# Kernel tuning notes

Hardware: AMD Instinct MI355X
Metric: run time of the kernel (lower is better)

The kernel has to match this reference:

```python
import jax, jax.numpy as jnp
import numpy as np
from functools import partial

H = 768          # hidden_size (bert-base)
S = 256          # seq_len, forced by pool Linear(256*H -> H)
V = 30522        # vocab_size
NUM_TAGS = 2
B = 32


def _lstm_layer(x, w_ih, w_hh, b_ih, b_hh):
    # x: (B, S, I); torch weight layout: w_ih (4H, I), w_hh (4H, H), gate order i,f,g,o
    b, _, _ = x.shape
    h0 = jnp.zeros((b, H), x.dtype)
    c0 = jnp.zeros((b, H), x.dtype)
    bias = b_ih + b_hh

    def step(carry, xt):
        h, c = carry
        gates = xt @ w_ih.T + h @ w_hh.T + bias          # (B, 4H)
        i, f, g, o = jnp.split(gates, 4, axis=-1)
        i = jax.nn.sigmoid(i)
        f = jax.nn.sigmoid(f)
        g = jnp.tanh(g)
        o = jax.nn.sigmoid(o)
        c = f * c + i * g
        h = o * jnp.tanh(c)
        return (h, c), h

    _, hs = jax.lax.scan(step, (h0, c0), x.transpose(1, 0, 2))  # hs: (S, B, H)
    return hs.transpose(1, 0, 2)


def setup_inputs() -> dict:
    key = jax.random.key(0)
    ks = jax.random.split(key, 16)
    sc = 0.02
    inp = {
        "input_ids": jax.random.randint(ks[0], (B, S), 0, V, dtype=jnp.int32),
        "attention_mask": jnp.ones((B, S), jnp.int32),
        "token_type_ids": jnp.zeros((B, S), jnp.int32),
        "seq_label": jax.random.randint(ks[1], (B, NUM_TAGS), 0, 2, dtype=jnp.int32),
        "entity_ids": jax.random.randint(ks[2], (B, S), 0, 2, dtype=jnp.int32),
        "embed_table": jax.random.normal(ks[3], (V, H), jnp.float32) * sc,
        "w_ih0": jax.random.normal(ks[4], (4 * H, H), jnp.float32) * sc,
        "w_hh0": jax.random.normal(ks[5], (4 * H, H), jnp.float32) * sc,
        "b_ih0": jnp.zeros((4 * H,), jnp.float32),
        "b_hh0": jnp.zeros((4 * H,), jnp.float32),
        "w_ih1": jax.random.normal(ks[6], (4 * H, H), jnp.float32) * sc,
        "w_hh1": jax.random.normal(ks[7], (4 * H, H), jnp.float32) * sc,
        "b_ih1": jnp.zeros((4 * H,), jnp.float32),
        "b_hh1": jnp.zeros((4 * H,), jnp.float32),
        "pool_w": jax.random.normal(ks[8], (S * H, H), jnp.float32) * 0.002,
        "pool_b": jnp.zeros((H,), jnp.float32),
        "lin_w": jax.random.normal(ks[9], (H, NUM_TAGS), jnp.float32) * sc,
        "lin_b": jnp.zeros((NUM_TAGS,), jnp.float32),
    }
    return inp


def reference(input_ids, attention_mask, token_type_ids, seq_label, entity_ids,
              embed_table, w_ih0, w_hh0, b_ih0, b_hh0, w_ih1, w_hh1, b_ih1, b_hh1,
              pool_w, pool_b, lin_w, lin_b):
    x = embed_table[input_ids]                              # (B, S, H)
    out = _lstm_layer(x, w_ih0, w_hh0, b_ih0, b_hh0)        # layer 1
    out = _lstm_layer(out, w_ih1, w_hh1, b_ih1, b_hh1)      # layer 2 -> (B, S, H)

    seq_out = out.reshape(out.shape[0], -1) @ pool_w + pool_b   # (B, H)

    # batched version of the per-sample loop:
    # entity_out = tokens * (entity_ids == 1); concat seq_out row; global max over tokens
    mask = (entity_ids == 1).astype(out.dtype)[:, :, None]      # (B, S, 1)
    entity_out = out * mask                                     # (B, S, H)
    batch_out = jnp.maximum(entity_out.max(axis=1), seq_out)    # adaptive_max_pool1d(size=1)

    logits = batch_out @ lin_w + lin_b                          # (B, num_tags)

    # BCEWithLogitsLoss (dropout in eval mode = identity), numerically stable
    y = seq_label.astype(logits.dtype)
    loss = jnp.mean(jnp.maximum(logits, 0) - logits * y + jnp.log1p(jnp.exp(-jnp.abs(logits))))
    return (loss, logits)
```

## Files before the change

kernel.cpp:

```cpp
#include <hip/hip_runtime.h>
#include <hip/hip_bf16.h>
#include <stdint.h>

constexpr int Hh  = 768;
constexpr int Ss  = 256;
constexpr int Bb  = 32;
constexpr int NWGL = 96;
constexpr int UPW8 = Hh / NWGL;
constexpr int LCW  = 4 * UPW8;
constexpr int WPAD = Hh + 8;
constexpr int CPT  = 256;
constexpr int PB   = 40;
constexpr int NCH  = 3;

typedef short bf16x8 __attribute__((ext_vector_type(8)));
typedef float f32x4  __attribute__((ext_vector_type(4)));
typedef float f32x2  __attribute__((ext_vector_type(2)));
typedef uint32_t u32x4 __attribute__((ext_vector_type(4)));

__device__ __forceinline__ unsigned short f2bf(float f) {
  union { float f; uint32_t u; } v; v.f = f;
  uint32_t u = v.u;
  return (unsigned short)((u + 0x7FFFu + ((u >> 16) & 1u)) >> 16);
}
__device__ __forceinline__ float bf2f(unsigned short h) {
  union { uint32_t u; float f; } v; v.u = ((uint32_t)h) << 16; return v.f;
}

__global__ __launch_bounds__(256) void k_embed(const int* __restrict__ ids,
                                               const float* __restrict__ table,
                                               unsigned short* __restrict__ x_bf) {
  int row = blockIdx.x;
  int b = row / Ss, s = row - b * Ss;
  int id  = ids[row];
  const float* src = table + (size_t)id * Hh;
  unsigned short* dst = x_bf + ((size_t)s * Bb + b) * Hh;
  for (int j = threadIdx.x; j < Hh; j += 256) dst[j] = f2bf(src[j]);
}

__global__ __launch_bounds__(256) void k_lstm2(
    const unsigned short* __restrict__ x_bf,
    const float* __restrict__ w_ih0, const float* __restrict__ w_hh0,
    const float* __restrict__ w_ih1, const float* __restrict__ w_hh1,
    const float* __restrict__ b_ih0, const float* __restrict__ b_hh0,
    const float* __restrict__ b_ih1, const float* __restrict__ b_hh1,
    unsigned short* __restrict__ hseq1,
    unsigned short* __restrict__ hseq2,
    unsigned int* __restrict__ sync) {
  __shared__ __align__(16) unsigned short Whh[LCW * WPAD];
  __shared__ __align__(16) unsigned short Wih[LCW * WPAD];
  __shared__ __align__(16) unsigned short hbuf[2][16][8];
  __shared__ __align__(16) float gsum[2][2][16][33];
  __shared__ int prodf[2], consf[2];
  __shared__ int stepC, stepP;

  const int wgid = blockIdx.x;
  const int tid = threadIdx.x;
  const int lane = tid & 63, w = tid >> 6;
  unsigned int* cnt1 = sync;
  unsigned int* cnt2 = sync + Ss * CPT;

  const int layer = wgid >= NWGL;
  const int wg = layer ? wgid - NWGL : wgid;
  const int u0 = wg * UPW8;
  const int bkt = wg & 15;

  if (tid < 2) { prodf[tid] = 0; consf[tid] = -1; }
  if (tid == 2) stepC = 0;
  if (tid == 3) stepP = 0;

  {
    const float* whsrc = layer ? w_hh1 : w_hh0;
    const float* wisrc = layer ? w_ih1 : w_ih0;
    for (int cch = tid; cch < LCW * 96; cch += 256) {
      int row = cch / 96, kc = cch - row * 96;
      int gi = row >> 3, u = row & 7;
      const float* sp = whsrc + ((size_t)gi * Hh + u0 + u) * Hh + kc * 8;
      float4 va = ((const float4*)sp)[0], vb = ((const float4*)sp)[1];
      bf16x8 pk;
      pk[0] = (short)f2bf(va.x); pk[1] = (short)f2bf(va.y);
      pk[2] = (short)f2bf(va.z); pk[3] = (short)f2bf(va.w);
      pk[4] = (short)f2bf(vb.x); pk[5] = (short)f2bf(vb.y);
      pk[6] = (short)f2bf(vb.z); pk[7] = (short)f2bf(vb.w);
      *(bf16x8*)&Whh[row * WPAD + kc * 8] = pk;
      const float* sp2 = wisrc + ((size_t)gi * Hh + u0 + u) * Hh + kc * 8;
      float4 vc = ((const float4*)sp2)[0], vd = ((const float4*)sp2)[1];
      bf16x8 pk2;
      pk2[0] = (short)f2bf(vc.x); pk2[1] = (short)f2bf(vc.y);
      pk2[2] = (short)f2bf(vc.z); pk2[3] = (short)f2bf(vc.w);
      pk2[4] = (short)f2bf(vd.x); pk2[5] = (short)f2bf(vd.y);
      pk2[6] = (short)f2bf(vd.z); pk2[7] = (short)f2bf(vd.w);
      *(bf16x8*)&Wih[row * WPAD + kc * 8] = pk2;
    }
  }
  __syncthreads();

  const int l15 = lane & 15, kq = lane >> 4;
  const bool lo8 = (l15 < 8);
  volatile int* scp = &stepC;
  volatile int* spp = &stepP;

  if (w >= 2) {
    const int bh = w - 2;
    const int brow = bh * 16 + l15;
    for (int t = 0; t < Ss; ++t) {
      if (layer) {
        if (w == 2) {
          const unsigned int* bk = cnt1 + (size_t)t * CPT;
          for (;;) {
            unsigned v = 12;
            if (lane < 16)
              v = __hip_atomic_load(bk + lane * 16, __ATOMIC_RELAXED, __HIP_MEMORY_SCOPE_AGENT);
            if (__all(v >= 12u)) break;
            __builtin_amdgcn_s_sleep(2);
          }
          asm volatile("" ::: "memory");
          if (lane == 0) *spp = t + 1;
          asm volatile("s_waitcnt lgkmcnt(0)" ::: "memory");
        } else {
          while (*spp < t + 1) __builtin_amdgcn_s_sleep(1);
          asm volatile("" ::: "memory");
        }
      }
      const unsigned short* ap = (layer ? hseq1 : x_bf)
                               + ((size_t)t * Bb + brow) * Hh + kq * 8;
      bf16x8 areg[24];
      #pragma unroll
      for (int kk = 0; kk < 24; ++kk) areg[kk] = *(const bf16x8*)(ap + kk * 32);
      f32x4 aI[2][2];
      #pragma unroll
      for (int nt = 0; nt < 2; ++nt) {
        aI[nt][0] = (f32x4){0.f,0.f,0.f,0.f}; aI[nt][1] = (f32x4){0.f,0.f,0.f,0.f};
        const int c = nt * 16 + l15;
        #pragma unroll
        for (int kk = 0; kk < 24; ++kk) {
          bf16x8 bfr = *(const bf16x8*)&Wih[c * WPAD + kk * 32 + kq * 8];
          aI[nt][kk & 1] = __builtin_amdgcn_mfma_f32_16x16x32_bf16(areg[kk], bfr, aI[nt][kk & 1], 0, 0, 0);
        }
      }
      while (__hip_atomic_load(&consf[bh], __ATOMIC_RELAXED, __HIP_MEMORY_SCOPE_WORKGROUP) < t - 1)
        __builtin_amdgcn_s_sleep(0);
      const int par = t & 1;
      #pragma unroll
      for (int nt = 0; nt < 2; ++nt)
        #pragma unroll
        for (int r = 0; r < 4; ++r)
          gsum[par][bh][kq * 4 + r][nt * 16 + l15] = aI[nt][0][r] + aI[nt][1][r];
      __hip_atomic_store(&prodf[bh], t + 1, __ATOMIC_RELEASE, __HIP_MEMORY_SCOPE_WORKGROUP);
    }
    return;
  }

  const int bh = w;
  const int brow = bh * 16 + l15;
  const float k1 = lo8 ? 2.f : 1.f;
  const float m1 = lo8 ? 2.f : 1.f;
  const float d1 = lo8 ? -1.f : 0.f;

  float bl[2];
  #pragma unroll
  for (int nt = 0; nt < 2; ++nt) {
    int c = nt * 16 + l15;
    int gcol = (c >> 3) * Hh + u0 + (c & 7);
    bl[nt] = layer ? (b_ih1[gcol] + b_hh1[gcol]) : (b_ih0[gcol] + b_hh0[gcol]);
  }

  float cc[4] = {0.f, 0.f, 0.f, 0.f};
  unsigned short* hout = layer ? hseq2 : hseq1;
  unsigned int* mycnt = layer ? cnt2 : cnt1;

  for (int t = 0; t < Ss; ++t) {
    f32x4 aW[2][2];
    #pragma unroll
    for (int nt = 0; nt < 2; ++nt) {
      aW[nt][0] = (f32x4){0.f,0.f,0.f,0.f}; aW[nt][1] = (f32x4){0.f,0.f,0.f,0.f};
    }
    if (t > 0) {
      if (w == 0) {
        const unsigned int* bown = mycnt + (size_t)(t - 1) * CPT;
        for (;;) {
          unsigned v = 12;
          if (lane < 16)
            v = __hip_atomic_load(bown + lane * 16, __ATOMIC_RELAXED, __HIP_MEMORY_SCOPE_AGENT);
          if (__all(v >= 12u)) break;
          __builtin_amdgcn_s_sleep(2);
        }
        asm volatile("" ::: "memory");
        if (lane == 0) *scp = t;
        asm volatile("s_waitcnt lgkmcnt(0)" ::: "memory");
      } else {
        while (*scp < t) __builtin_amdgcn_s_sleep(1);
        asm volatile("" ::: "memory");
      }
      const unsigned short* ap = hout + ((size_t)(t - 1) * Bb + brow) * Hh + kq * 8;
      bf16x8 areg[24];
      #pragma unroll
      for (int kk = 0; kk < 24; ++kk) areg[kk] = *(const bf16x8*)(ap + kk * 32);
      #pragma unroll
      for (int nt = 0; nt < 2; ++nt) {
        const int c = nt * 16 + l15;
        #pragma unroll
        for (int kk = 0; kk < 24; ++kk) {
          bf16x8 bfr = *(const bf16x8*)&Whh[c * WPAD + kk * 32 + kq * 8];
          aW[nt][kk & 1] = __builtin_amdgcn_mfma_f32_16x16x32_bf16(areg[kk], bfr, aW[nt][kk & 1], 0, 0, 0);
        }
      }
    }

    float gin[2][4];
    {
      while (__hip_atomic_load(&prodf[bh], __ATOMIC_ACQUIRE, __HIP_MEMORY_SCOPE_WORKGROUP) < t + 1)
        __builtin_amdgcn_s_sleep(0);
      const int par = t & 1;
      #pragma unroll
      for (int nt = 0; nt < 2; ++nt)
        #pragma unroll
        for (int r = 0; r < 4; ++r)
          gin[nt][r] = gsum[par][bh][kq * 4 + r][nt * 16 + l15] + bl[nt];
      __hip_atomic_store(&consf[bh], t, __ATOMIC_RELEASE, __HIP_MEMORY_SCOPE_WORKGROUP);
    }

    float act0[4], act1[4];
    #pragma unroll
    for (int r = 0; r < 4; ++r) {
      float v0 = aW[0][0][r] + aW[0][1][r] + gin[0][r];
      act0[r] = 1.f / (1.f + __expf(-v0));
      float v1 = aW[1][0][r] + aW[1][1][r] + gin[1][r];
      act1[r] = m1 / (1.f + __expf(-k1 * v1)) + d1;
    }

    #pragma unroll
    for (int r = 0; r < 4; ++r) {
      float p0 = __shfl_xor(act0[r], 8);
      float p1 = __shfl_xor(act1[r], 8);
      float iv = lo8 ? act0[r] : p0;
      float fv = lo8 ? p0 : act0[r];
      float gv = lo8 ? act1[r] : p1;
      float ov = lo8 ? p1 : act1[r];
      float cn = fv * cc[r] + iv * gv;
      cc[r] = cn;
      float e = __expf(-2.f * cn);
      float hv = ov * (1.f - e) / (1.f + e);
      if (lo8) hbuf[w][kq * 4 + r][l15] = f2bf(hv);
    }
    asm volatile("s_waitcnt lgkmcnt(0)" ::: "memory");

    if (lane < 16) {
      const unsigned long long* hb = (const unsigned long long*)&hbuf[w][lane][0];
      unsigned long long x0 = hb[0], x1 = hb[1];
      unsigned long long* hp =
          (unsigned long long*)(hout + ((size_t)t * Bb + (bh * 16 + lane)) * Hh + u0);
      __hip_atomic_store(hp + 0, x0, __ATOMIC_RELAXED, __HIP_MEMORY_SCOPE_AGENT);
      __hip_atomic_store(hp + 1, x1, __ATOMIC_RELAXED, __HIP_MEMORY_SCOPE_AGENT);
    }
    asm volatile("s_waitcnt vmcnt(0)" ::: "memory");
    if (lane == 0) {
      unsigned int* cp = mycnt + (size_t)t * CPT + bkt * 16;
      (void)__hip_atomic_fetch_add(cp, 1u, __ATOMIC_RELAXED, __HIP_MEMORY_SCOPE_AGENT);
    }
  }
}

__global__ __launch_bounds__(256) void k_pool_partial(const unsigned short* __restrict__ hseq2,
                                                      const float* __restrict__ pw,
                                                      float* __restrict__ partial) {
  __shared__ __align__(16) unsigned short osm[Hh * PB];
  const int tid = threadIdx.x;
  const int s = blockIdx.x, nc = blockIdx.y;
  for (int b = 0; b < Bb; ++b) {
    const unsigned short* src = hseq2 + ((size_t)s * Bb + b) * Hh;
    for (int k = tid; k < Hh; k += 256) osm[k * PB + b] = src[k];
  }
  __syncthreads();
  f32x2 acc[16];
  #pragma unroll
  for (int bp = 0; bp < 16; ++bp) acc[bp] = (f32x2){0.f, 0.f};
  const float* pbase = pw + (size_t)s * Hh * Hh + nc * 256 + tid;
  #pragma unroll 4
  for (int k = 0; k < Hh; ++k) {
    float wv = pbase[(size_t)k * Hh];
    u32x4 h0 = *(const u32x4*)&osm[k * PB + 0];
    u32x4 h1 = *(const u32x4*)&osm[k * PB + 8];
    u32x4 h2 = *(const u32x4*)&osm[k * PB + 16];
    u32x4 h3 = *(const u32x4*)&osm[k * PB + 24];
    uint32_t hw[16] = {h0[0],h0[1],h0[2],h0[3], h1[0],h1[1],h1[2],h1[3],
                       h2[0],h2[1],h2[2],h2[3], h3[0],h3[1],h3[2],h3[3]};
    #pragma unroll
    for (int bp = 0; bp < 16; ++bp) {
      uint32_t pv = hw[bp];
      f32x2 ov;
      ov.x = __uint_as_float(pv << 16);
      ov.y = __uint_as_float(pv & 0xffff0000u);
      acc[bp] += ov * wv;
    }
  }
  float* pout = partial + (size_t)(s * NCH + nc) * (Bb * 256);
  #pragma unroll
  for (int bp = 0; bp < 16; ++bp) {
    pout[(size_t)(bp * 2 + 0) * 256 + tid] = acc[bp].x;
    pout[(size_t)(bp * 2 + 1) * 256 + tid] = acc[bp].y;
  }
}

__global__ __launch_bounds__(256) void k_pool_reduce(const float* __restrict__ partial,
                                                     const float* __restrict__ pool_b,
                                                     float* __restrict__ seq_out) {
  int i = blockIdx.x * 256 + threadIdx.x;
  int b = i / Hh, n = i - b * Hh;
  int nchunk = n >> 8, nn = n & 255;
  float acc = pool_b[n];
  const float* p = partial + (size_t)nchunk * (Bb * 256) + b * 256 + nn;
  #pragma unroll 8
  for (int t = 0; t < Ss; ++t) acc += p[(size_t)t * NCH * (Bb * 256)];
  seq_out[i] = acc;
}

__global__ __launch_bounds__(256) void k_entity_logits(const unsigned short* __restrict__ hseq2,
                                                       const float* __restrict__ seq_out,
                                                       const int* __restrict__ entity_ids,
                                                       const float* __restrict__ lin_w,
                                                       const float* __restrict__ lin_b,
                                                       float* __restrict__ logits_ws,
                                                       float* __restrict__ dlogits) {
  const int b = blockIdx.x, tid = threadIdx.x;
  float m0 = -1e30f, m1 = -1e30f, m2 = -1e30f;
  for (int s = 0; s < Ss; ++s) {
    bool e = entity_ids[b * Ss + s] == 1;
    const unsigned short* row = hseq2 + ((size_t)s * Bb + b) * Hh;
    float v0 = bf2f(row[tid]);
    float v1 = bf2f(row[256 + tid]);
    float v2 = bf2f(row[512 + tid]);
    v0 = e ? v0 : 0.f; v1 = e ? v1 : 0.f; v2 = e ? v2 : 0.f;
    m0 = fmaxf(m0, v0); m1 = fmaxf(m1, v1); m2 = fmaxf(m2, v2);
  }
  __shared__ float red[512];
  float p0 = 0.f, p1 = 0.f;
  float mm[3] = {m0, m1, m2};
  #pragma unroll
  for (int j = 0; j < 3; ++j) {
    int n = j * 256 + tid;
    float bo = fmaxf(mm[j], seq_out[b * Hh + n]);
    p0 += bo * lin_w[n * 2 + 0];
    p1 += bo * lin_w[n * 2 + 1];
  }
  red[tid] = p0; red[256 + tid] = p1;
  __syncthreads();
  for (int off = 128; off > 0; off >>= 1) {
    if (tid < off) { red[tid] += red[tid + off]; red[256 + tid] += red[256 + tid + off]; }
    __syncthreads();
  }
  if (tid == 0) {
    float l0 = red[0] + lin_b[0], l1 = red[256] + lin_b[1];
    logits_ws[b * 2] = l0; logits_ws[b * 2 + 1] = l1;
    dlogits[b * 2] = l0;  dlogits[b * 2 + 1] = l1;
  }
}

__global__ void k_loss(const float* __restrict__ logits, const int* __restrict__ lab,
                       float* __restrict__ dout) {
  __shared__ float red[64];
  int i = threadIdx.x;
  float l = logits[i];
  float y = (float)lab[i];
  red[i] = fmaxf(l, 0.f) - l * y + log1pf(__expf(-fabsf(l)));
  __syncthreads();
  for (int off = 32; off > 0; off >>= 1) {
    if (i < off) red[i] += red[i + off];
    __syncthreads();
  }
  if (i == 0) dout[0] = red[0] * (1.f / 64.f);
}

extern "C" void kernel_launch(void* const* d_in, const int* in_sizes, int n_in,
                              void* d_out, int out_size, void* d_ws, size_t ws_size,
                              hipStream_t stream) {
  const int*   input_ids  = (const int*)d_in[0];
  const int*   seq_label  = (const int*)d_in[3];
  const int*   entity_ids = (const int*)d_in[4];
  const float* embed      = (const float*)d_in[5];
  const float* w_ih0      = (const float*)d_in[6];
  const float* w_hh0      = (const float*)d_in[7];
  const float* b_ih0      = (const float*)d_in[8];
  const float* b_hh0      = (const float*)d_in[9];
  const float* w_ih1      = (const float*)d_in[10];
  const float* w_hh1      = (const float*)d_in[11];
  const float* b_ih1      = (const float*)d_in[12];
  const float* b_hh1      = (const float*)d_in[13];
  const float* pool_w     = (const float*)d_in[14];
  const float* pool_b     = (const float*)d_in[15];
  const float* lin_w      = (const float*)d_in[16];
  const float* lin_b      = (const float*)d_in[17];
  float* out = (float*)d_out;

  const size_t SZ_XO = (size_t)Bb * Ss * Hh * 2;
  const size_t SZ_SY = (size_t)2 * Ss * CPT * 4;
  char* ws = (char*)d_ws;
  size_t off = 0;
  unsigned short* x_bf   = (unsigned short*)(ws + off); off += SZ_XO;
  unsigned short* hseq1  = (unsigned short*)(ws + off); off += SZ_XO;
  unsigned short* hseq2  = (unsigned short*)(ws + off); off += SZ_XO;
  float*          seq_out= (float*)(ws + off);          off += (size_t)Bb * Hh * 4;
  float*          logits = (float*)(ws + off);          off += 1024;
  unsigned int*   syncb  = (unsigned int*)(ws + off);   off += SZ_SY;
  float*          partial = (float*)ws;

  hipMemsetAsync(syncb, 0, SZ_SY, stream);

  k_embed<<<Bb * Ss, 256, 0, stream>>>(input_ids, embed, x_bf);

  k_lstm2<<<2 * NWGL, 256, 0, stream>>>(x_bf, w_ih0, w_hh0, w_ih1, w_hh1,
                                        b_ih0, b_hh0, b_ih1, b_hh1,
                                        hseq1, hseq2, syncb);

  dim3 pgrid(Ss, NCH);
  k_pool_partial<<<pgrid, 256, 0, stream>>>(hseq2, pool_w, partial);
  k_pool_reduce<<<(Bb * Hh) / 256, 256, 0, stream>>>(partial, pool_b, seq_out);
  k_entity_logits<<<Bb, 256, 0, stream>>>(hseq2, seq_out, entity_ids, lin_w, lin_b,
                                          logits, out + 1);
  k_loss<<<1, 64, 0, stream>>>(logits, seq_label, out);
}
```

Before: 2.193 ms.

## Add dedicated polling wave for cross-WG sync and fuse pool-reduce/loss into logits

Adds a fifth wavefront per workgroup that solely polls the global step counters and publishes progress to LDS flags. The compute waves then spin on LDS with minimal sleep instead of one compute wave doing the global polling. Separately, the pool reduction and loss kernels are folded into the entity/logits kernel, with a last-block atomic counter computing the loss, which removes two launches. The cost is extra threads per block and a serial partial-sum reduction inside only 32 blocks.

```diff
diff --git a/kernel.cpp b/kernel.cpp
--- a/kernel.cpp
+++ b/kernel.cpp
@@ -38,7 +38,7 @@
   for (int j = threadIdx.x; j < Hh; j += 256) dst[j] = f2bf(src[j]);
 }
 
-__global__ __launch_bounds__(256) void k_lstm2(
+__global__ __launch_bounds__(320) void k_lstm2(
     const unsigned short* __restrict__ x_bf,
     const float* __restrict__ w_ih0, const float* __restrict__ w_hh0,
     const float* __restrict__ w_ih1, const float* __restrict__ w_hh1,
@@ -72,7 +72,7 @@
   {
     const float* whsrc = layer ? w_hh1 : w_hh0;
     const float* wisrc = layer ? w_ih1 : w_ih0;
-    for (int cch = tid; cch < LCW * 96; cch += 256) {
+    for (int cch = tid; cch < LCW * 96; cch += 320) {
       int row = cch / 96, kc = cch - row * 96;
       int gi = row >> 3, u = row & 7;
       const float* sp = whsrc + ((size_t)gi * Hh + u0 + u) * Hh + kc * 8;
@@ -99,28 +99,51 @@
   const bool lo8 = (l15 < 8);
   volatile int* scp = &stepC;
   volatile int* spp = &stepP;
+  unsigned int* mycnt = layer ? cnt2 : cnt1;
+
+  if (w == 4) {
+    if (layer) {
+      int tc = 1, tp = 0;
+      while (tc <= Ss || tp < Ss) {
+        bool c = true;
+        if (lane < 16 && tc <= Ss)
+          c = __hip_atomic_load(cnt2 + (size_t)(tc - 1) * CPT + lane * 16,
+                                __ATOMIC_RELAXED, __HIP_MEMORY_SCOPE_AGENT) >= 12u;
+        else if (lane >= 16 && lane < 32 && tp < Ss)
+          c = __hip_atomic_load(cnt1 + (size_t)tp * CPT + (lane - 16) * 16,
+                                __ATOMIC_RELAXED, __HIP_MEMORY_SCOPE_AGENT) >= 12u;
+        unsigned long long bal = __ballot(c);
+        bool ownok = (tc <= Ss) && ((bal & 0xFFFFull) == 0xFFFFull);
+        bool inok  = (tp < Ss) && (((bal >> 16) & 0xFFFFull) == 0xFFFFull);
+        asm volatile("" ::: "memory");
+        if (ownok) { if (lane == 0) *scp = tc; ++tc; }
+        if (inok)  { if (lane == 0) *spp = tp + 1; ++tp; }
+        if (!ownok && !inok) __builtin_amdgcn_s_sleep(1);
+      }
+    } else {
+      for (int tc = 1; tc <= Ss; ++tc) {
+        for (;;) {
+          unsigned v = 12;
+          if (lane < 16)
+            v = __hip_atomic_load(cnt1 + (size_t)(tc - 1) * CPT + lane * 16,
+                                  __ATOMIC_RELAXED, __HIP_MEMORY_SCOPE_AGENT);
+          if (__all(v >= 12u)) break;
+          __builtin_amdgcn_s_sleep(1);
+        }
+        asm volatile("" ::: "memory");
+        if (lane == 0) *scp = tc;
+      }
+    }
+    return;
+  }
 
   if (w >= 2) {
     const int bh = w - 2;
     const int brow = bh * 16 + l15;
     for (int t = 0; t < Ss; ++t) {
       if (layer) {
-        if (w == 2) {
-          const unsigned int* bk = cnt1 + (size_t)t * CPT;
-          for (;;) {
-            unsigned v = 12;
-            if (lane < 16)
-              v = __hip_atomic_load(bk + lane * 16, __ATOMIC_RELAXED, __HIP_MEMORY_SCOPE_AGENT);
-            if (__all(v >= 12u)) break;
-            __builtin_amdgcn_s_sleep(2);
-          }
-          asm volatile("" ::: "memory");
-          if (lane == 0) *spp = t + 1;
-          asm volatile("s_waitcnt lgkmcnt(0)" ::: "memory");
-        } else {
-          while (*spp < t + 1) __builtin_amdgcn_s_sleep(1);
-          asm volatile("" ::: "memory");
-        }
+        while (*spp < t + 1) __builtin_amdgcn_s_sleep(0);
+        asm volatile("" ::: "memory");
       }
       const unsigned short* ap = (layer ? hseq1 : x_bf)
                                + ((size_t)t * Bb + brow) * Hh + kq * 8;
@@ -167,7 +190,6 @@
 
   float cc[4] = {0.f, 0.f, 0.f, 0.f};
   unsigned short* hout = layer ? hseq2 : hseq1;
-  unsigned int* mycnt = layer ? cnt2 : cnt1;
 
   for (int t = 0; t < Ss; ++t) {
     f32x4 aW[2][2];
@@ -176,22 +198,8 @@
       aW[nt][0] = (f32x4){0.f,0.f,0.f,0.f}; aW[nt][1] = (f32x4){0.f,0.f,0.f,0.f};
     }
     if (t > 0) {
-      if (w == 0) {
-        const unsigned int* bown = mycnt + (size_t)(t - 1) * CPT;
-        for (;;) {
-          unsigned v = 12;
-          if (lane < 16)
-            v = __hip_atomic_load(bown + lane * 16, __ATOMIC_RELAXED, __HIP_MEMORY_SCOPE_AGENT);
-          if (__all(v >= 12u)) break;
-          __builtin_amdgcn_s_sleep(2);
-        }
-        asm volatile("" ::: "memory");
-        if (lane == 0) *scp = t;
-        asm volatile("s_waitcnt lgkmcnt(0)" ::: "memory");
-      } else {
-        while (*scp < t) __builtin_amdgcn_s_sleep(1);
-        asm volatile("" ::: "memory");
-      }
+      while (*scp < t) __builtin_amdgcn_s_sleep(0);
+      asm volatile("" ::: "memory");
       const unsigned short* ap = hout + ((size_t)(t - 1) * Bb + brow) * Hh + kq * 8;
       bf16x8 areg[24];
       #pragma unroll
@@ -302,26 +310,16 @@
   }
 }
 
-__global__ __launch_bounds__(256) void k_pool_reduce(const float* __restrict__ partial,
-                                                     const float* __restrict__ pool_b,
-                                                     float* __restrict__ seq_out) {
-  int i = blockIdx.x * 256 + threadIdx.x;
-  int b = i / Hh, n = i - b * Hh;
-  int nchunk = n >> 8, nn = n & 255;
-  float acc = pool_b[n];
-  const float* p = partial + (size_t)nchunk * (Bb * 256) + b * 256 + nn;
-  #pragma unroll 8
-  for (int t = 0; t < Ss; ++t) acc += p[(size_t)t * NCH * (Bb * 256)];
-  seq_out[i] = acc;
-}
-
 __global__ __launch_bounds__(256) void k_entity_logits(const unsigned short* __restrict__ hseq2,
-                                                       const float* __restrict__ seq_out,
+                                                       const float* __restrict__ partial,
+                                                       const float* __restrict__ pool_b,
                                                        const int* __restrict__ entity_ids,
                                                        const float* __restrict__ lin_w,
                                                        const float* __restrict__ lin_b,
+                                                       const int* __restrict__ seq_label,
                                                        float* __restrict__ logits_ws,
-                                                       float* __restrict__ dlogits) {
+                                                       unsigned int* __restrict__ done,
+                                                       float* __restrict__ out) {
   const int b = blockIdx.x, tid = threadIdx.x;
   float m0 = -1e30f, m1 = -1e30f, m2 = -1e30f;
   for (int s = 0; s < Ss; ++s) {
@@ -333,16 +331,20 @@
     v0 = e ? v0 : 0.f; v1 = e ? v1 : 0.f; v2 = e ? v2 : 0.f;
     m0 = fmaxf(m0, v0); m1 = fmaxf(m1, v1); m2 = fmaxf(m2, v2);
   }
-  __shared__ float red[512];
+  float mm[3] = {m0, m1, m2};
   float p0 = 0.f, p1 = 0.f;
-  float mm[3] = {m0, m1, m2};
   #pragma unroll
   for (int j = 0; j < 3; ++j) {
     int n = j * 256 + tid;
-    float bo = fmaxf(mm[j], seq_out[b * Hh + n]);
+    float acc = pool_b[n];
+    const float* p = partial + (size_t)j * (Bb * 256) + b * 256 + tid;
+    #pragma unroll 8
+    for (int s = 0; s < Ss; ++s) acc += p[(size_t)s * NCH * (Bb * 256)];
+    float bo = fmaxf(mm[j], acc);
     p0 += bo * lin_w[n * 2 + 0];
     p1 += bo * lin_w[n * 2 + 1];
   }
+  __shared__ float red[512];
   red[tid] = p0; red[256 + tid] = p1;
   __syncthreads();
   for (int off = 128; off > 0; off >>= 1) {
@@ -351,24 +353,20 @@
   }
   if (tid == 0) {
     float l0 = red[0] + lin_b[0], l1 = red[256] + lin_b[1];
-    logits_ws[b * 2] = l0; logits_ws[b * 2 + 1] = l1;
-    dlogits[b * 2] = l0;  dlogits[b * 2 + 1] = l1;
-  }
-}
-
-__global__ void k_loss(const float* __restrict__ logits, const int* __restrict__ lab,
-                       float* __restrict__ dout) {
-  __shared__ float red[64];
-  int i = threadIdx.x;
-  float l = logits[i];
-  float y = (float)lab[i];
-  red[i] = fmaxf(l, 0.f) - l * y + log1pf(__expf(-fabsf(l)));
-  __syncthreads();
-  for (int off = 32; off > 0; off >>= 1) {
-    if (i < off) red[i] += red[i + off];
-    __syncthreads();
-  }
-  if (i == 0) dout[0] = red[0] * (1.f / 64.f);
+    out[1 + b * 2] = l0; out[1 + b * 2 + 1] = l1;
+    __hip_atomic_store(logits_ws + b * 2 + 0, l0, __ATOMIC_RELAXED, __HIP_MEMORY_SCOPE_AGENT);
+    __hip_atomic_store(logits_ws + b * 2 + 1, l1, __ATOMIC_RELAXED, __HIP_MEMORY_SCOPE_AGENT);
+    unsigned d = __hip_atomic_fetch_add(done, 1u, __ATOMIC_ACQ_REL, __HIP_MEMORY_SCOPE_AGENT);
+    if (d == (unsigned)(Bb - 1)) {
+      float s = 0.f;
+      for (int i = 0; i < 2 * Bb; ++i) {
+        float l = __hip_atomic_load(logits_ws + i, __ATOMIC_RELAXED, __HIP_MEMORY_SCOPE_AGENT);
+        float y = (float)seq_label[i];
+        s += fmaxf(l, 0.f) - l * y + log1pf(__expf(-fabsf(l)));
+      }
+      out[0] = s * (1.f / (2.f * Bb));
+    }
+  }
 }
 
 extern "C" void kernel_launch(void* const* d_in, const int* in_sizes, int n_in,
@@ -393,29 +391,27 @@
   float* out = (float*)d_out;
 
   const size_t SZ_XO = (size_t)Bb * Ss * Hh * 2;
-  const size_t SZ_SY = (size_t)2 * Ss * CPT * 4;
+  const size_t SZ_SY = (size_t)(2 * Ss * CPT + 64) * 4;
   char* ws = (char*)d_ws;
   size_t off = 0;
   unsigned short* x_bf   = (unsigned short*)(ws + off); off += SZ_XO;
   unsigned short* hseq1  = (unsigned short*)(ws + off); off += SZ_XO;
   unsigned short* hseq2  = (unsigned short*)(ws + off); off += SZ_XO;
-  float*          seq_out= (float*)(ws + off);          off += (size_t)Bb * Hh * 4;
   float*          logits = (float*)(ws + off);          off += 1024;
   unsigned int*   syncb  = (unsigned int*)(ws + off);   off += SZ_SY;
+  unsigned int*   done   = syncb + 2 * Ss * CPT;
   float*          partial = (float*)ws;
 
   hipMemsetAsync(syncb, 0, SZ_SY, stream);
 
   k_embed<<<Bb * Ss, 256, 0, stream>>>(input_ids, embed, x_bf);
 
-  k_lstm2<<<2 * NWGL, 256, 0, stream>>>(x_bf, w_ih0, w_hh0, w_ih1, w_hh1,
+  k_lstm2<<<2 * NWGL, 320, 0, stream>>>(x_bf, w_ih0, w_hh0, w_ih1, w_hh1,
                                         b_ih0, b_hh0, b_ih1, b_hh1,
                                         hseq1, hseq2, syncb);
 
   dim3 pgrid(Ss, NCH);
   k_pool_partial<<<pgrid, 256, 0, stream>>>(hseq2, pool_w, partial);
-  k_pool_reduce<<<(Bb * Hh) / 256, 256, 0, stream>>>(partial, pool_b, seq_out);
-  k_entity_logits<<<Bb, 256, 0, stream>>>(hseq2, seq_out, entity_ids, lin_w, lin_b,
-                                          logits, out + 1);
-  k_loss<<<1, 64, 0, stream>>>(logits, seq_label, out);
-}
+  k_entity_logits<<<Bb, 256, 0, stream>>>(hseq2, partial, pool_b, entity_ids,
+                                          lin_w, lin_b, seq_label, logits, done, out);
+}
```

Result: slower. 2.431 ms (+10.9%).

## Replace store-drain before counter increment with sentinel-verified reads of hidden state

Applied to the files above, without the earlier changes.

Removes the vmcnt(0) wait between the hidden-state stores and the counter atomic increment, so producers signal without waiting for their stores to complete. Both hidden-state buffers are pre-filled with 0xFF sentinels. Consumers check the loaded bf16 values for the sentinel and re-poll with atomic loads until real data shows up. This takes the store-completion latency off the serial recurrence critical path. In exchange it adds two 12.6MB memsets per call, a per-load sentinel check, and a correctness risk if a real bf16 value ever equals 0xFFFF or if only half of a 16-byte write is visible.

```diff
diff --git a/kernel.cpp b/kernel.cpp
--- a/kernel.cpp
+++ b/kernel.cpp
@@ -25,6 +25,31 @@
 }
 __device__ __forceinline__ float bf2f(unsigned short h) {
   union { uint32_t u; float f; } v; v.u = ((uint32_t)h) << 16; return v.f;
+}
+
+__device__ __forceinline__ void load_verified(const unsigned short* ap, bf16x8 (&areg)[24]) {
+  #pragma unroll
+  for (int kk = 0; kk < 24; ++kk) areg[kk] = *(const bf16x8*)(ap + kk * 32);
+  for (;;) {
+    bool bad = false;
+    #pragma unroll
+    for (int kk = 0; kk < 24; ++kk) {
+      unsigned lo0 = (unsigned)(unsigned short)areg[kk][0];
+      unsigned lo4 = (unsigned)(unsigned short)areg[kk][4];
+      bad = bad || (lo0 == 0xFFFFu) || (lo4 == 0xFFFFu);
+    }
+    if (!__any(bad)) return;
+    const unsigned long long* pp = (const unsigned long long*)ap;
+    #pragma unroll
+    for (int kk = 0; kk < 24; ++kk) {
+      unsigned long long q0 = __hip_atomic_load(pp + kk * 8,     __ATOMIC_RELAXED, __HIP_MEMORY_SCOPE_AGENT);
+      unsigned long long q1 = __hip_atomic_load(pp + kk * 8 + 1, __ATOMIC_RELAXED, __HIP_MEMORY_SCOPE_AGENT);
+      union { unsigned long long q[2]; bf16x8 v; } u;
+      u.q[0] = q0; u.q[1] = q1;
+      areg[kk] = u.v;
+    }
+    __builtin_amdgcn_s_sleep(0);
+  }
 }
 
 __global__ __launch_bounds__(256) void k_embed(const int* __restrict__ ids,
@@ -122,11 +147,14 @@
           asm volatile("" ::: "memory");
         }
       }
-      const unsigned short* ap = (layer ? hseq1 : x_bf)
-                               + ((size_t)t * Bb + brow) * Hh + kq * 8;
       bf16x8 areg[24];
-      #pragma unroll
-      for (int kk = 0; kk < 24; ++kk) areg[kk] = *(const bf16x8*)(ap + kk * 32);
+      if (layer) {
+        load_verified(hseq1 + ((size_t)t * Bb + brow) * Hh + kq * 8, areg);
+      } else {
+        const unsigned short* ap = x_bf + ((size_t)t * Bb + brow) * Hh + kq * 8;
+        #pragma unroll
+        for (int kk = 0; kk < 24; ++kk) areg[kk] = *(const bf16x8*)(ap + kk * 32);
+      }
       f32x4 aI[2][2];
       #pragma unroll
       for (int nt = 0; nt < 2; ++nt) {
@@ -192,10 +220,8 @@
         while (*scp < t) __builtin_amdgcn_s_sleep(1);
         asm volatile("" ::: "memory");
       }
-      const unsigned short* ap = hout + ((size_t)(t - 1) * Bb + brow) * Hh + kq * 8;
       bf16x8 areg[24];
-      #pragma unroll
-      for (int kk = 0; kk < 24; ++kk) areg[kk] = *(const bf16x8*)(ap + kk * 32);
+      load_verified(hout + ((size_t)(t - 1) * Bb + brow) * Hh + kq * 8, areg);
       #pragma unroll
       for (int nt = 0; nt < 2; ++nt) {
         const int c = nt * 16 + l15;
@@ -253,7 +279,6 @@
       __hip_atomic_store(hp + 0, x0, __ATOMIC_RELAXED, __HIP_MEMORY_SCOPE_AGENT);
       __hip_atomic_store(hp + 1, x1, __ATOMIC_RELAXED, __HIP_MEMORY_SCOPE_AGENT);
     }
-    asm volatile("s_waitcnt vmcnt(0)" ::: "memory");
     if (lane == 0) {
       unsigned int* cp = mycnt + (size_t)t * CPT + bkt * 16;
       (void)__hip_atomic_fetch_add(cp, 1u, __ATOMIC_RELAXED, __HIP_MEMORY_SCOPE_AGENT);
@@ -405,6 +430,8 @@
   float*          partial = (float*)ws;
 
   hipMemsetAsync(syncb, 0, SZ_SY, stream);
+  hipMemsetAsync(hseq1, 0xFF, SZ_XO, stream);
+  hipMemsetAsync(hseq2, 0xFF, SZ_XO, stream);
 
   k_embed<<<Bb * Ss, 256, 0, stream>>>(input_ids, embed, x_bf);
 
```

After: 2.267 ms. +3.4%, slower.
